# Kernel tuning notes

Measured on AMD Instinct MI355X. Metric: run time of the kernel, lower is better.

## Reference

```python
import jax, jax.numpy as jnp
import numpy as np

RATIO = 0.6
ROT_FACTOR = 0.1  # fraction of 2*pi
B, H, W, C = 32, 512, 512, 3
S = 2 * max(H, W)  # mask side = 2*max(H, W) = 1024
FILL_VALUE = 1  # source references undefined self.fill_value; stripes are set to 1


def setup_inputs() -> dict:
    key = jax.random.key(0)
    k1, k2 = jax.random.split(key)
    images = jax.random.uniform(k1, (B, H, W, C), jnp.float32) * 255.0
    max_ang = ROT_FACTOR * 2.0 * np.pi
    angles = jax.random.uniform(k2, (B,), jnp.float32, -max_ang, max_ang)
    rng = np.random.default_rng(0)
    lo = int(min(H * 0.5, W * 0.3))
    hi = int(max(H * 0.5, W * 0.3))
    gridblock = rng.integers(lo, hi + 1, size=B).astype(np.int32)
    start1 = rng.integers(0, gridblock + 1).astype(np.int32)  # uniform [0, gridblock]
    start2 = rng.integers(0, gridblock + 1).astype(np.int32)
    return {
        "images": images,
        "angles": angles,
        "gridblock": jnp.asarray(gridblock),
        "start1": jnp.asarray(start1),
        "start2": jnp.asarray(start2),
    }


def _build_masks(gridblock, start1, start2):
    # Vectorized equivalent of the nested scatter loops: mask[i,j] = 1 iff
    # row i is in a stripe (pass 1) OR column j is in a stripe (pass 2).
    gb = gridblock[:, None].astype(jnp.int32)  # [B,1]
    length = jnp.clip((gb.astype(jnp.float32) * RATIO + 0.5).astype(jnp.int32), 1, gb - 1)
    n = S // gb  # number of stripes per image
    r = jnp.arange(S, dtype=jnp.int32)[None, :]  # [1,S]

    def stripes(start):
        d = r - start[:, None]
        return (d >= 0) & (jnp.mod(d, gb) < length) & ((d // gb) < n)

    rows = stripes(start1)  # [B,S]
    cols = stripes(start2)  # [B,S]
    return (rows[:, :, None] | cols[:, None, :]).astype(jnp.float32)  # [B,S,S]


def _rotate_bilinear_reflect(mask, angles):
    # Rotate each mask about its center by angles[b] (CCW), bilinear interp,
    # reflect fill (TF 'reflect': d c b a | a b c d | d c b a).
    c = (S - 1) / 2.0
    yy, xx = jnp.meshgrid(jnp.arange(S, dtype=jnp.float32),
                          jnp.arange(S, dtype=jnp.float32), indexing="ij")
    cos = jnp.cos(angles)[:, None, None]
    sin = jnp.sin(angles)[:, None, None]
    x = xx[None] - c
    y = yy[None] - c
    sx = cos * x + sin * y + c  # inverse-map source coords [B,S,S]
    sy = -sin * x + cos * y + c
    x0 = jnp.floor(sx)
    y0 = jnp.floor(sy)
    fx = sx - x0
    fy = sy - y0
    x0i = x0.astype(jnp.int32)
    y0i = y0.astype(jnp.int32)

    def refl(i):
        m = jnp.mod(i, 2 * S)
        return jnp.where(m < S, m, 2 * S - 1 - m)

    x0r, x1r = refl(x0i), refl(x0i + 1)
    y0r, y1r = refl(y0i), refl(y0i + 1)
    b = jnp.arange(mask.shape[0])[:, None, None]
    v00 = mask[b, y0r, x0r]
    v01 = mask[b, y0r, x1r]
    v10 = mask[b, y1r, x0r]
    v11 = mask[b, y1r, x1r]
    return (v00 * (1 - fx) * (1 - fy) + v01 * fx * (1 - fy)
            + v10 * (1 - fx) * fy + v11 * fx * fy)


def reference(images, angles, gridblock, start1, start2):
    mask = _build_masks(gridblock, start1, start2) * FILL_VALUE  # [B,S,S]
    rot = _rotate_bilinear_reflect(mask, angles)
    off_h = (S - H) // 2
    off_w = (S - W) // 2
    m = rot[:, off_h:off_h + H, off_w:off_w + W]  # center crop [B,H,W]
    return images * m[..., None]
```

## Files before the change

### kernel.cpp

```cpp
#include <hip/hip_runtime.h>

namespace {
constexpr int S = 1024;
constexpr int B = 32;
constexpr int OFF = 256;

typedef float f32x4 __attribute__((ext_vector_type(4)));

__device__ __forceinline__ float stripef(int i, int start, int gb, int len, int n, float inv_gb) {
    const int d = i - start;
    int q = (int)((float)d * inv_gb);
    int r = d - q * gb;
    if (r < 0)        { r += gb; --q; }
    else if (r >= gb) { r -= gb; ++q; }
    return (d >= 0 && r < len && q < n) ? 1.0f : 0.0f;
}

__global__ __launch_bounds__(512) void gridmask_kernel(
    const float* __restrict__ images,
    const float* __restrict__ angles,
    const int* __restrict__ gridblock,
    const int* __restrict__ start1,
    const int* __restrict__ start2,
    float* __restrict__ out)
{
    __shared__ float2 colsAD[1024];
    __shared__ float2 rowsAD[1024];
    __shared__ float  mlds[4096];

    const int tid = threadIdx.x;
    const int blk = blockIdx.x;
    const int b   = blk >> 6;
    const int y0  = (blk & 63) << 3;

    const size_t fbase = (size_t)blk * 12288;
    const float4* __restrict__ gin4 = (const float4*)(images + fbase);
    float4 p[6];
#pragma unroll
    for (int j = 0; j < 6; ++j) p[j] = gin4[(j << 9) + tid];

    const float ang = angles[b];
    const int gb = gridblock[b];
    const int s1 = start1[b];
    const int s2 = start2[b];

    const float gbf = (float)gb;
    int len = (int)(__fadd_rn(__fmul_rn(gbf, 0.6f), 0.5f));
    len = min(max(len, 1), gb - 1);
    const int n = S / gb;
    const float inv_gb = 1.0f / gbf;

    {
        const int i0 = tid << 1;
        const float r0 = stripef(i0,     s1, gb, len, n, inv_gb);
        const float r1 = stripef(i0 + 1, s1, gb, len, n, inv_gb);
        const float r2 = stripef(i0 + 2, s1, gb, len, n, inv_gb);
        rowsAD[i0]     = make_float2(r0, r1 - r0);
        rowsAD[i0 + 1] = make_float2(r1, r2 - r1);
        const float c0 = stripef(i0,     s2, gb, len, n, inv_gb);
        const float c1 = stripef(i0 + 1, s2, gb, len, n, inv_gb);
        const float c2 = stripef(i0 + 2, s2, gb, len, n, inv_gb);
        colsAD[i0]     = make_float2(c0, c1 - c0);
        colsAD[i0 + 1] = make_float2(c1, c2 - c1);
    }
    __syncthreads();

    {
        float sn, cs;
        sincosf(ang, &sn, &cs);
        const float c = (float)(S - 1) * 0.5f;
        const float X = (float)(tid + OFF) - c;
#pragma unroll
        for (int r = 0; r < 8; ++r) {
            const float Yr = (float)(y0 + r + OFF) - c;
            const float sx = cs * X + sn * Yr + c;
            const float sy = cs * Yr - sn * X + c;
            const float x0f = floorf(sx);
            const float y0f = floorf(sy);
            const float fx = sx - x0f;
            const float fy = sy - y0f;
            const int xi = (int)x0f;
            const int yi = (int)y0f;
            const float2 cad = colsAD[xi];
            const float2 rad = rowsAD[yi];
            const float cx = fmaf(fx, cad.y, cad.x);
            const float ry = fmaf(fy, rad.y, rad.x);
            mlds[(r << 9) + tid] = cx + ry - cx * ry;
        }
    }
    __syncthreads();

    f32x4* __restrict__ gout4 = (f32x4*)(out + fbase);
#pragma unroll
    for (int j = 0; j < 6; ++j) {
        const int lf = (j << 11) + (tid << 2);
        const int q  = lf / 3;
        const int r  = lf - q * 3;
        const float ma = mlds[q];
        const float mb = mlds[min(q + 1, 4095)];
        const float m0 = ma;
        const float m1 = (r + 1 >= 3) ? mb : ma;
        const float m2 = (r + 2 >= 3) ? mb : ma;
        const float m3 = (r + 3 >= 3) ? mb : ma;
        f32x4 o;
        o.x = p[j].x * m0;
        o.y = p[j].y * m1;
        o.z = p[j].z * m2;
        o.w = p[j].w * m3;
        __builtin_nontemporal_store(o, gout4 + (j << 9) + tid);
    }
}
}

extern "C" void kernel_launch(void* const* d_in, const int* in_sizes, int n_in,
                              void* d_out, int out_size, void* d_ws, size_t ws_size,
                              hipStream_t stream) {
    const float* images    = (const float*)d_in[0];
    const float* angles    = (const float*)d_in[1];
    const int*   gridblock = (const int*)d_in[2];
    const int*   start1    = (const int*)d_in[3];
    const int*   start2    = (const int*)d_in[4];
    float* outp = (float*)d_out;

    gridmask_kernel<<<2048, 512, 0, stream>>>(images, angles, gridblock, start1, start2, outp);
}
```

Before: 183.1 us.

## Split fused gridmask into separate mask-generation and multiply kernels via workspace

Replaces the single fused kernel with two launches. The first builds the rotated, cropped mask for all images into a workspace buffer. The second streams the images and multiplies them by the mask with a flat, grid-strided access pattern. The aim is to decouple mask computation from the bandwidth-bound multiply and drop the per-block stripe rebuild. The cost is an extra 32 MB mask write and read plus a second launch. The old fused kernel stays as a fallback when no workspace is available.

```diff
diff --git a/kernel.cpp b/kernel.cpp
--- a/kernel.cpp
+++ b/kernel.cpp
@@ -4,6 +4,9 @@
 constexpr int S = 1024;
 constexpr int B = 32;
 constexpr int OFF = 256;
+constexpr int NPIX = B * 512 * 512;
+constexpr int NF4  = NPIX * 3 / 4;
+constexpr size_t MASK_BYTES = (size_t)NPIX * 4;
 
 typedef float f32x4 __attribute__((ext_vector_type(4)));
 
@@ -14,6 +17,116 @@
     if (r < 0)        { r += gb; --q; }
     else if (r >= gb) { r -= gb; ++q; }
     return (d >= 0 && r < len && q < n) ? 1.0f : 0.0f;
+}
+
+__global__ __launch_bounds__(256) void mask_kernel(
+    const float* __restrict__ angles,
+    const int* __restrict__ gridblock,
+    const int* __restrict__ start1,
+    const int* __restrict__ start2,
+    float* __restrict__ mask)
+{
+    __shared__ float2 colsAD[1024];
+    __shared__ float2 rowsAD[1024];
+
+    const int tid = threadIdx.x;
+    const int img = blockIdx.x >> 4;
+    const int seg = blockIdx.x & 15;
+
+    const float ang = angles[img];
+    const int gb = gridblock[img];
+    const int s1 = start1[img];
+    const int s2 = start2[img];
+
+    const float gbf = (float)gb;
+    int len = (int)(__fadd_rn(__fmul_rn(gbf, 0.6f), 0.5f));
+    len = min(max(len, 1), gb - 1);
+    const int n = S / gb;
+    const float inv_gb = 1.0f / gbf;
+
+    {
+        const int i0 = tid << 2;
+        float rv[5], cv[5];
+#pragma unroll
+        for (int i = 0; i < 5; ++i) {
+            rv[i] = stripef(i0 + i, s1, gb, len, n, inv_gb);
+            cv[i] = stripef(i0 + i, s2, gb, len, n, inv_gb);
+        }
+#pragma unroll
+        for (int i = 0; i < 4; ++i) {
+            rowsAD[i0 + i] = make_float2(rv[i], rv[i + 1] - rv[i]);
+            colsAD[i0 + i] = make_float2(cv[i], cv[i + 1] - cv[i]);
+        }
+    }
+    __syncthreads();
+
+    float sn, cs;
+    sincosf(ang, &sn, &cs);
+    const float c = (float)(S - 1) * 0.5f;
+
+    float4* __restrict__ mask4 = (float4*)mask + (size_t)img * 65536 + (size_t)seg * 4096;
+
+#pragma unroll
+    for (int k = 0; k < 16; ++k) {
+        const int f4  = (k << 8) + tid;
+        const int pix = (((seg << 12) + f4) << 2);
+        const int y = pix >> 9;
+        const int x = pix & 511;
+        const float Y = (float)(y + OFF) - c;
+        float m[4];
+#pragma unroll
+        for (int i = 0; i < 4; ++i) {
+            const float X  = (float)(x + i + OFF) - c;
+            const float sx = cs * X + sn * Y + c;
+            const float sy = cs * Y - sn * X + c;
+            const float x0f = floorf(sx);
+            const float y0f = floorf(sy);
+            const float fx = sx - x0f;
+            const float fy = sy - y0f;
+            const float2 cad = colsAD[(int)x0f];
+            const float2 rad = rowsAD[(int)y0f];
+            const float cx = fmaf(fx, cad.y, cad.x);
+            const float ry = fmaf(fy, rad.y, rad.x);
+            m[i] = cx + ry - cx * ry;
+        }
+        mask4[f4] = make_float4(m[0], m[1], m[2], m[3]);
+    }
+}
+
+__global__ __launch_bounds__(256) void mul_kernel(
+    const float* __restrict__ images,
+    const float* __restrict__ mask,
+    float* __restrict__ out)
+{
+    const int t = blockIdx.x * 256 + threadIdx.x;
+    const float4* __restrict__ in4 = (const float4*)images;
+    f32x4* __restrict__ out4 = (f32x4*)out;
+
+    float4 p[6];
+    float ma[6], mb[6];
+    int r3[6];
+#pragma unroll
+    for (int j = 0; j < 6; ++j) {
+        const int idx = t + (j << 20);
+        p[j] = in4[idx];
+        const unsigned lf = (unsigned)idx << 2;
+        const unsigned q = __umulhi(lf, 0xAAAAAAABu) >> 1;
+        r3[j] = (int)(lf - q * 3u);
+        ma[j] = mask[q];
+        mb[j] = mask[q + 1];
+    }
+#pragma unroll
+    for (int j = 0; j < 6; ++j) {
+        const int idx = t + (j << 20);
+        const float m1 = (r3[j] == 2) ? mb[j] : ma[j];
+        const float m2 = (r3[j] != 0) ? mb[j] : ma[j];
+        f32x4 o;
+        o.x = p[j].x * ma[j];
+        o.y = p[j].y * m1;
+        o.z = p[j].z * m2;
+        o.w = p[j].w * mb[j];
+        __builtin_nontemporal_store(o, out4 + idx);
+    }
 }
 
 __global__ __launch_bounds__(512) void gridmask_kernel(
@@ -79,10 +192,8 @@
             const float y0f = floorf(sy);
             const float fx = sx - x0f;
             const float fy = sy - y0f;
-            const int xi = (int)x0f;
-            const int yi = (int)y0f;
-            const float2 cad = colsAD[xi];
-            const float2 rad = rowsAD[yi];
+            const float2 cad = colsAD[(int)x0f];
+            const float2 rad = rowsAD[(int)y0f];
             const float cx = fmaf(fx, cad.y, cad.x);
             const float ry = fmaf(fy, rad.y, rad.x);
             mlds[(r << 9) + tid] = cx + ry - cx * ry;
@@ -122,5 +233,11 @@
     const int*   start2    = (const int*)d_in[4];
     float* outp = (float*)d_out;
 
-    gridmask_kernel<<<2048, 512, 0, stream>>>(images, angles, gridblock, start1, start2, outp);
-}
+    if (d_ws != nullptr && ws_size >= MASK_BYTES) {
+        float* maskp = (float*)d_ws;
+        mask_kernel<<<512, 256, 0, stream>>>(angles, gridblock, start1, start2, maskp);
+        mul_kernel<<<NF4 / (6 * 256), 256, 0, stream>>>(images, maskp, outp);
+    } else {
+        gridmask_kernel<<<2048, 512, 0, stream>>>(images, angles, gridblock, start1, start2, outp);
+    }
+}
```

After: 201.3 us. +9.9%, slower.

## Compute mask per output vector directly, drop LDS mask stage and halve block size

Applied to the files above, without the earlier changes.

Each thread now computes the rotated mask values for the two pixels its float4 spans, which removes the shared-memory mask staging and the second barrier. Blocks shrink to 256 threads with twice as many launched, and each thread builds four entries of the row and column stripe tables. Stores change from nontemporal to ordinary. The cost is redundant mask computation (two per float4, each pixel about 1.33 times) and losing the nontemporal hint on a streaming output.

```diff
diff --git a/kernel.cpp b/kernel.cpp
--- a/kernel.cpp
+++ b/kernel.cpp
@@ -16,7 +16,7 @@
     return (d >= 0 && r < len && q < n) ? 1.0f : 0.0f;
 }
 
-__global__ __launch_bounds__(512) void gridmask_kernel(
+__global__ __launch_bounds__(256) void gridmask_kernel(
     const float* __restrict__ images,
     const float* __restrict__ angles,
     const int* __restrict__ gridblock,
@@ -26,18 +26,16 @@
 {
     __shared__ float2 colsAD[1024];
     __shared__ float2 rowsAD[1024];
-    __shared__ float  mlds[4096];
 
     const int tid = threadIdx.x;
     const int blk = blockIdx.x;
-    const int b   = blk >> 6;
-    const int y0  = (blk & 63) << 3;
+    const int b   = blk >> 7;
 
-    const size_t fbase = (size_t)blk * 12288;
-    const float4* __restrict__ gin4 = (const float4*)(images + fbase);
+    const size_t f4base = (size_t)b * 196608 + (size_t)(blk & 127) * 1536;
+    const float4* __restrict__ gin4 = (const float4*)images + f4base;
     float4 p[6];
 #pragma unroll
-    for (int j = 0; j < 6; ++j) p[j] = gin4[(j << 9) + tid];
+    for (int j = 0; j < 6; ++j) p[j] = gin4[(j << 8) + tid];
 
     const float ang = angles[b];
     const int gb = gridblock[b];
@@ -51,63 +49,64 @@
     const float inv_gb = 1.0f / gbf;
 
     {
-        const int i0 = tid << 1;
-        const float r0 = stripef(i0,     s1, gb, len, n, inv_gb);
-        const float r1 = stripef(i0 + 1, s1, gb, len, n, inv_gb);
-        const float r2 = stripef(i0 + 2, s1, gb, len, n, inv_gb);
-        rowsAD[i0]     = make_float2(r0, r1 - r0);
-        rowsAD[i0 + 1] = make_float2(r1, r2 - r1);
-        const float c0 = stripef(i0,     s2, gb, len, n, inv_gb);
-        const float c1 = stripef(i0 + 1, s2, gb, len, n, inv_gb);
-        const float c2 = stripef(i0 + 2, s2, gb, len, n, inv_gb);
-        colsAD[i0]     = make_float2(c0, c1 - c0);
-        colsAD[i0 + 1] = make_float2(c1, c2 - c1);
+        const int i0 = tid << 2;
+        float rv[5], cv[5];
+#pragma unroll
+        for (int i = 0; i < 5; ++i) {
+            rv[i] = stripef(i0 + i, s1, gb, len, n, inv_gb);
+            cv[i] = stripef(i0 + i, s2, gb, len, n, inv_gb);
+        }
+#pragma unroll
+        for (int i = 0; i < 4; ++i) {
+            rowsAD[i0 + i] = make_float2(rv[i], rv[i + 1] - rv[i]);
+            colsAD[i0 + i] = make_float2(cv[i], cv[i + 1] - cv[i]);
+        }
     }
     __syncthreads();
 
-    {
-        float sn, cs;
-        sincosf(ang, &sn, &cs);
-        const float c = (float)(S - 1) * 0.5f;
-        const float X = (float)(tid + OFF) - c;
+    float sn, cs;
+    sincosf(ang, &sn, &cs);
+    const float c = (float)(S - 1) * 0.5f;
+
+    const unsigned wbase = ((unsigned)(blk & 127) * 1536u) << 2;
+
+    f32x4* __restrict__ gout4 = (f32x4*)out + f4base;
+
 #pragma unroll
-        for (int r = 0; r < 8; ++r) {
-            const float Yr = (float)(y0 + r + OFF) - c;
-            const float sx = cs * X + sn * Yr + c;
-            const float sy = cs * Yr - sn * X + c;
+    for (int j = 0; j < 6; ++j) {
+        const int lf4 = (j << 8) + tid;
+        const unsigned wlf = wbase + ((unsigned)lf4 << 2);
+        const unsigned q = __umulhi(wlf, 0xAAAAAAABu) >> 1;
+        const int r = (int)(wlf - q * 3u);
+        float mm[2];
+#pragma unroll
+        for (int k = 0; k < 2; ++k) {
+            const unsigned qq = q + (unsigned)k;
+            const int y = (int)(qq >> 9);
+            const int x = (int)(qq & 511u);
+            const float X = (float)(x + OFF) - c;
+            const float Y = (float)(y + OFF) - c;
+            const float sx = cs * X + sn * Y + c;
+            const float sy = cs * Y - sn * X + c;
             const float x0f = floorf(sx);
             const float y0f = floorf(sy);
             const float fx = sx - x0f;
             const float fy = sy - y0f;
-            const int xi = (int)x0f;
-            const int yi = (int)y0f;
-            const float2 cad = colsAD[xi];
-            const float2 rad = rowsAD[yi];
-            const float cx = fmaf(fx, cad.y, cad.x);
-            const float ry = fmaf(fy, rad.y, rad.x);
-            mlds[(r << 9) + tid] = cx + ry - cx * ry;
+            const float2 cad = colsAD[(int)x0f];
+            const float2 rad = rowsAD[(int)y0f];
+            const float cxv = fmaf(fx, cad.y, cad.x);
+            const float ryv = fmaf(fy, rad.y, rad.x);
+            mm[k] = cxv + ryv - cxv * ryv;
         }
-    }
-    __syncthreads();
-
-    f32x4* __restrict__ gout4 = (f32x4*)(out + fbase);
-#pragma unroll
-    for (int j = 0; j < 6; ++j) {
-        const int lf = (j << 11) + (tid << 2);
-        const int q  = lf / 3;
-        const int r  = lf - q * 3;
-        const float ma = mlds[q];
-        const float mb = mlds[min(q + 1, 4095)];
-        const float m0 = ma;
-        const float m1 = (r + 1 >= 3) ? mb : ma;
-        const float m2 = (r + 2 >= 3) ? mb : ma;
-        const float m3 = (r + 3 >= 3) ? mb : ma;
+        const float ma = mm[0], mb = mm[1];
+        const float m1 = (r == 2) ? mb : ma;
+        const float m2 = (r != 0) ? mb : ma;
         f32x4 o;
-        o.x = p[j].x * m0;
+        o.x = p[j].x * ma;
         o.y = p[j].y * m1;
         o.z = p[j].z * m2;
-        o.w = p[j].w * m3;
-        __builtin_nontemporal_store(o, gout4 + (j << 9) + tid);
+        o.w = p[j].w * mb;
+        gout4[lf4] = o;
     }
 }
 }
@@ -122,5 +121,5 @@
     const int*   start2    = (const int*)d_in[4];
     float* outp = (float*)d_out;
 
-    gridmask_kernel<<<2048, 512, 0, stream>>>(images, angles, gridblock, start1, start2, outp);
+    gridmask_kernel<<<4096, 256, 0, stream>>>(images, angles, gridblock, start1, start2, outp);
 }
```

After: 184.5 us. About the same (+0.8%).
